# Optimization experiments

Measured on AMD Instinct MI355X. Metric: run time of the kernel, lower is better.

## Reference

```python
import jax, jax.numpy as jnp
import numpy as np

N, E, IN_DIM, HID, HEADS, OUT_DIM, MAX_N = 40000, 200000, 32, 64, 4, 32, 8
SLOPE = 0.2  # GATv2Conv default negative_slope


def setup_inputs() -> dict:
    key = jax.random.key(0)
    ks = jax.random.split(key, 10)
    s = lambda k, shape: jax.random.normal(k, shape, dtype=jnp.float32) * 0.1
    return {
        "feat": jax.random.normal(ks[0], (N, IN_DIM), dtype=jnp.float32),
        "edge_index": jax.random.randint(ks[1], (2, E), 0, N, dtype=jnp.int32),
        # edge_mask values in 1..MAX_N so max().item() == MAX_N as in the torch loop
        "edge_mask": jax.random.randint(ks[2], (E,), 1, MAX_N + 1, dtype=jnp.int32),
        "current_state": jnp.ones((N,), dtype=jnp.bool_),
        "W_in": s(ks[3], (HID, IN_DIM)), "b_in": jnp.zeros((HID,), jnp.float32),
        "W_l": s(ks[4], (HEADS * HID, 2 * HID)), "b_l": jnp.zeros((HEADS * HID,), jnp.float32),
        "W_r": s(ks[5], (HEADS * HID, 2 * HID)), "b_r": jnp.zeros((HEADS * HID,), jnp.float32),
        "att": s(ks[6], (HEADS, HID)),
        "b_conv": jnp.zeros((HEADS * HID,), jnp.float32),
        "W_g": s(ks[7], (OUT_DIM, HID)), "b_g": jnp.zeros((OUT_DIM,), jnp.float32),
    }


def _gatv2(x, src, dst, emask, W_l, b_l, W_r, b_r, att, b_conv):
    """GATv2Conv(2*HID -> HID, heads=HEADS, add_self_loops=False) on masked edges."""
    xl = (x @ W_l.T + b_l).reshape(N, HEADS, HID)  # source transform
    xr = (x @ W_r.T + b_r).reshape(N, HEADS, HID)  # target transform
    e = jax.nn.leaky_relu(xl[src] + xr[dst], SLOPE)          # (E, heads, hid)
    logits = jnp.einsum('ehd,hd->eh', e, att)                # (E, heads)
    logits = jnp.where(emask[:, None], logits, -1e9)
    seg_max = jax.ops.segment_max(logits, dst, num_segments=N)
    w = jnp.exp(logits - seg_max[dst]) * emask[:, None].astype(logits.dtype)
    denom = jax.ops.segment_sum(w, dst, num_segments=N)
    alpha = w / jnp.maximum(denom[dst], 1e-16)               # scatter-softmax over dst
    out = jax.ops.segment_sum(xl[src] * alpha[:, :, None], dst, num_segments=N)
    return out + b_conv.reshape(HEADS, HID)                  # (N, heads, hid)


def reference(feat, edge_index, edge_mask, current_state, W_in, b_in,
              W_l, b_l, W_r, b_r, att, b_conv, W_g, b_g):
    src, dst = edge_index[0], edge_index[1]
    h0 = feat @ W_in.T + b_in
    h = h0
    temp = jnp.zeros_like(h)
    for i in range(MAX_N):  # max_n = edge_mask.max() == MAX_N by construction
        emask = i < edge_mask
        conv = _gatv2(jnp.concatenate([h, h0], axis=1), src, dst, emask,
                      W_l, b_l, W_r, b_r, att, b_conv)
        h = jnp.tanh(conv.sum(axis=1))         # view(N, heads, hid).sum(1) then tanh
        temp = jnp.where(h != 0, h, temp)      # temp[nonzero_mask] = h[nonzero_mask]
    hg = temp[current_state]                   # all-ones mask -> (N, HID)
    return hg @ W_g.T + b_g
```

## Files before the change

### kernel.cpp

```cpp
#include <hip/hip_runtime.h>
#include <math.h>

#define HID 64
#define HEADS 4
#define IN_DIM 32
#define OUT_DIM 32
#define MAX_ITERS 8
#define SLOPE 0.2f

typedef __attribute__((ext_vector_type(8))) short short8;
typedef __attribute__((ext_vector_type(4))) float floatx4;

__device__ inline ushort f2bf(float x) {
    union { float f; uint u; } c;
    c.f = x;
    uint u = c.u;
    return (ushort)((u + 0x7fffu + ((u >> 16) & 1u)) >> 16);
}

__global__ void k_prepw(const float* __restrict__ W_l, const float* __restrict__ W_r,
                        short* __restrict__ Wb) {
    int idx = blockIdx.x * blockDim.x + threadIdx.x;
    if (idx >= 512 * 128) return;
    int o = idx >> 7, k = idx & 127;
    float v = (o < 256) ? W_l[o * 128 + k] : W_r[(o - 256) * 128 + k];
    int bn = o >> 4, olo = o & 15, ks = k >> 5, kq = (k >> 3) & 3, j = k & 7;
    int lane = kq * 16 + olo;
    Wb[(((bn * 4 + ks) * 64 + lane) << 3) + j] = (short)f2bf(v);
}

__global__ void k_prepw2(const float* __restrict__ W_in, const float* __restrict__ W_g,
                         float* __restrict__ WTin, float* __restrict__ WTg) {
    int idx = blockIdx.x * blockDim.x + threadIdx.x;
    if (idx < HID * IN_DIM) {
        int k = idx >> 6, j = idx & 63;
        WTin[idx] = W_in[j * IN_DIM + k];
    } else if (idx < 2 * HID * IN_DIM) {
        int i2 = idx - HID * IN_DIM;
        int k = i2 >> 5, j = i2 & 31;
        WTg[i2] = W_g[j * HID + k];
    }
}

__global__ void k_h0(const float4* __restrict__ feat4, const float* __restrict__ WTin,
                     const float* __restrict__ b_in, ushort* __restrict__ h0b,
                     ushort* __restrict__ hb, int n_nodes) {
    int idx = blockIdx.x * blockDim.x + threadIdx.x;
    if (idx >= n_nodes * HID) return;
    int node = idx >> 6, j = idx & 63;
    const float4* f4 = feat4 + (size_t)node * 8;
    float acc = b_in[j];
#pragma unroll
    for (int kk = 0; kk < 8; ++kk) {
        float4 f = f4[kk];
        acc = fmaf(f.x, WTin[(kk * 4 + 0) * 64 + j], acc);
        acc = fmaf(f.y, WTin[(kk * 4 + 1) * 64 + j], acc);
        acc = fmaf(f.z, WTin[(kk * 4 + 2) * 64 + j], acc);
        acc = fmaf(f.w, WTin[(kk * 4 + 3) * 64 + j], acc);
    }
    ushort b = f2bf(acc);
    h0b[idx] = b;
    hb[idx] = b;
}

__global__ void k_count2(const int* __restrict__ dst, const int* __restrict__ emask,
                         int* __restrict__ deg2, int E) {
    int e = blockIdx.x * blockDim.x + threadIdx.x;
    if (e < E) atomicAdd(&deg2[dst[e] * 8 + (8 - emask[e])], 1);
}

__global__ __launch_bounds__(256) void k_scanA(const int* __restrict__ deg2,
                                               int* __restrict__ node_excl,
                                               int* __restrict__ blk_sum, int n_nodes) {
    __shared__ int sh[256];
    int t = threadIdx.x;
    int n = blockIdx.x * 256 + t;
    int d = 0;
    if (n < n_nodes) {
        const int4* p = (const int4*)(deg2 + (size_t)n * 8);
        int4 a = p[0], b = p[1];
        d = a.x + a.y + a.z + a.w + b.x + b.y + b.z + b.w;
    }
    sh[t] = d;
    __syncthreads();
    for (int off = 1; off < 256; off <<= 1) {
        int u = (t >= off) ? sh[t - off] : 0;
        __syncthreads();
        sh[t] += u;
        __syncthreads();
    }
    if (n < n_nodes) node_excl[n] = sh[t] - d;
    if (t == 255) blk_sum[blockIdx.x] = sh[255];
}

__global__ void k_scanB(int* __restrict__ blk_sum, int nblk) {
    __shared__ int sh[256];
    int t = threadIdx.x;
    int v = (t < nblk) ? blk_sum[t] : 0;
    sh[t] = v;
    __syncthreads();
    for (int off = 1; off < 256; off <<= 1) {
        int u = (t >= off) ? sh[t - off] : 0;
        __syncthreads();
        sh[t] += u;
        __syncthreads();
    }
    if (t < nblk) blk_sum[t] = sh[t] - v;
}

__global__ __launch_bounds__(256) void k_scanC(const int* __restrict__ deg2,
                                               const int* __restrict__ node_excl,
                                               const int* __restrict__ blk_sum,
                                               int* __restrict__ Sb, int* __restrict__ cur,
                                               int n_nodes) {
    int n = blockIdx.x * 256 + threadIdx.x;
    if (n >= n_nodes) return;
    int base = blk_sum[blockIdx.x] + node_excl[n];
    const int4* p = (const int4*)(deg2 + (size_t)n * 8);
    int4 a = p[0], b = p[1];
    int c[8] = {a.x, a.y, a.z, a.w, b.x, b.y, b.z, b.w};
    int run = base;
#pragma unroll
    for (int q = 0; q < 8; ++q) {
        Sb[n * 8 + q] = run;
        cur[n * 8 + q] = run;
        run += c[q];
    }
    if (n == n_nodes - 1) Sb[n_nodes * 8] = run;
}

__global__ void k_fill2(const int* __restrict__ src, const int* __restrict__ dst,
                        const int* __restrict__ emask, int* __restrict__ cur,
                        int* __restrict__ csr_src, int E) {
    int e = blockIdx.x * blockDim.x + threadIdx.x;
    if (e >= E) return;
    int pos = atomicAdd(&cur[dst[e] * 8 + (8 - emask[e])], 1);
    csr_src[pos] = src[e];
}

__global__ __launch_bounds__(256) void k_transform_mfma(
    const ushort* __restrict__ hb, const ushort* __restrict__ h0b,
    const short* __restrict__ Wb,
    const float* __restrict__ b_l, const float* __restrict__ b_r,
    float* __restrict__ xl, float* __restrict__ xr, int n_nodes) {
    __shared__ ushort As[64][136];
    int bm = blockIdx.x;
    int t = threadIdx.x;
#pragma unroll
    for (int i = 0; i < 4; ++i) {
        int idx = t + i * 256;
        int row = idx >> 4, ch = idx & 15;
        int node = bm * 64 + row;
        uint4 v = make_uint4(0, 0, 0, 0);
        if (node < n_nodes) {
            const uint4* p = (ch < 8) ? (const uint4*)(hb + (size_t)node * 64)
                                      : (const uint4*)(h0b + (size_t)node * 64);
            v = p[ch & 7];
        }
        *(uint4*)&As[row][ch * 8] = v;
    }
    __syncthreads();

    int wave = t >> 6, lane = t & 63;
    int olo = lane & 15, quad = lane >> 4;

    short8 nfrag[4][4];
#pragma unroll
    for (int ks = 0; ks < 4; ++ks)
#pragma unroll
        for (int sm = 0; sm < 4; ++sm)
            nfrag[ks][sm] = *(const short8*)&As[sm * 16 + olo][ks * 32 + quad * 8];

#pragma unroll
    for (int bn = 0; bn < 8; ++bn) {
        int cb = bn * 4 + wave;
        int o0 = cb * 16 + quad * 4;
        float4 bias = (o0 < 256) ? *(const float4*)&b_l[o0]
                                 : *(const float4*)&b_r[o0 - 256];

        floatx4 acc[4];
#pragma unroll
        for (int sm = 0; sm < 4; ++sm) acc[sm] = (floatx4){0.f, 0.f, 0.f, 0.f};

        const short8* WbF = (const short8*)Wb + (size_t)cb * 4 * 64;
#pragma unroll
        for (int ks = 0; ks < 4; ++ks) {
            short8 wfrag = WbF[ks * 64 + lane];
#pragma unroll
            for (int sm = 0; sm < 4; ++sm)
                acc[sm] = __builtin_amdgcn_mfma_f32_16x16x32_bf16(wfrag, nfrag[ks][sm], acc[sm], 0, 0, 0);
        }
#pragma unroll
        for (int sm = 0; sm < 4; ++sm) {
            int node = bm * 64 + sm * 16 + olo;
            if (node < n_nodes) {
                float4 v = make_float4(acc[sm][0] + bias.x, acc[sm][1] + bias.y,
                                       acc[sm][2] + bias.z, acc[sm][3] + bias.w);
                if (o0 < 256) *(float4*)&xl[(size_t)node * 256 + o0] = v;
                else          *(float4*)&xr[(size_t)node * 256 + (o0 - 256)] = v;
            }
        }
    }
}

__device__ inline void edge_ls(const float4* __restrict__ xl4, int s, int lane,
                               const float4& r4, const float4& at,
                               float4& a, float& ts) {
    a = xl4[(size_t)s * 64 + lane];
    float vx = a.x + r4.x; vx = fmaxf(vx, SLOPE * vx);
    float vy = a.y + r4.y; vy = fmaxf(vy, SLOPE * vy);
    float vz = a.z + r4.z; vz = fmaxf(vz, SLOPE * vz);
    float vw = a.w + r4.w; vw = fmaxf(vw, SLOPE * vw);
    ts = fmaf(vx, at.x, fmaf(vy, at.y, fmaf(vz, at.z, vw * at.w)));
}

__global__ __launch_bounds__(256) void k_fused(
    const float4* __restrict__ xl4, const float4* __restrict__ xr4,
    const int* __restrict__ Sb, const int* __restrict__ csr_src,
    const float4* __restrict__ att4, const float* __restrict__ b_conv,
    ushort* __restrict__ hb, float* __restrict__ temp, int iter, int n_nodes) {
    int gid = blockIdx.x * blockDim.x + threadIdx.x;
    int n = __builtin_amdgcn_readfirstlane(gid >> 6);
    int lane = threadIdx.x & 63;
    if (n >= n_nodes) return;
    int p0 = Sb[n * 8];
    int p1 = Sb[n * 8 + (8 - iter)];

    float ax = 0.f, ay = 0.f, az = 0.f, aw = 0.f, denom = 0.f;
    if (p1 > p0) {
        float4 at = att4[lane];
        float4 r4 = xr4[(size_t)n * 64 + lane];
        int p = p0;
        for (; p + 4 <= p1; p += 4) {
            int s0 = csr_src[p], s1 = csr_src[p + 1], s2 = csr_src[p + 2], s3 = csr_src[p + 3];
            float4 a0, a1, a2, a3;
            float ts0, ts1, ts2, ts3;
            edge_ls(xl4, s0, lane, r4, at, a0, ts0);
            edge_ls(xl4, s1, lane, r4, at, a1, ts1);
            edge_ls(xl4, s2, lane, r4, at, a2, ts2);
            edge_ls(xl4, s3, lane, r4, at, a3, ts3);
            ts0 += __shfl_xor(ts0, 1); ts1 += __shfl_xor(ts1, 1);
            ts2 += __shfl_xor(ts2, 1); ts3 += __shfl_xor(ts3, 1);
            ts0 += __shfl_xor(ts0, 2); ts1 += __shfl_xor(ts1, 2);
            ts2 += __shfl_xor(ts2, 2); ts3 += __shfl_xor(ts3, 2);
            ts0 += __shfl_xor(ts0, 4); ts1 += __shfl_xor(ts1, 4);
            ts2 += __shfl_xor(ts2, 4); ts3 += __shfl_xor(ts3, 4);
            ts0 += __shfl_xor(ts0, 8); ts1 += __shfl_xor(ts1, 8);
            ts2 += __shfl_xor(ts2, 8); ts3 += __shfl_xor(ts3, 8);
            float w0 = __expf(ts0), w1 = __expf(ts1), w2 = __expf(ts2), w3 = __expf(ts3);
            denom += (w0 + w1) + (w2 + w3);
            ax = fmaf(w0, a0.x, fmaf(w1, a1.x, fmaf(w2, a2.x, fmaf(w3, a3.x, ax))));
            ay = fmaf(w0, a0.y, fmaf(w1, a1.y, fmaf(w2, a2.y, fmaf(w3, a3.y, ay))));
            az = fmaf(w0, a0.z, fmaf(w1, a1.z, fmaf(w2, a2.z, fmaf(w3, a3.z, az))));
            aw = fmaf(w0, a0.w, fmaf(w1, a1.w, fmaf(w2, a2.w, fmaf(w3, a3.w, aw))));
        }
        for (; p < p1; ++p) {
            int s = csr_src[p];
            float4 a;
            float ts;
            edge_ls(xl4, s, lane, r4, at, a, ts);
            ts += __shfl_xor(ts, 1);
            ts += __shfl_xor(ts, 2);
            ts += __shfl_xor(ts, 4);
            ts += __shfl_xor(ts, 8);
            float w = __expf(ts);
            denom += w;
            ax = fmaf(w, a.x, ax); ay = fmaf(w, a.y, ay);
            az = fmaf(w, a.z, az); aw = fmaf(w, a.w, aw);
        }
        float inv = 1.f / fmaxf(denom, 1e-16f);
        ax *= inv; ay *= inv; az *= inv; aw *= inv;
        ax += __shfl_xor(ax, 16); ay += __shfl_xor(ay, 16);
        az += __shfl_xor(az, 16); aw += __shfl_xor(aw, 16);
        ax += __shfl_xor(ax, 32); ay += __shfl_xor(ay, 32);
        az += __shfl_xor(az, 32); aw += __shfl_xor(aw, 32);
    }
    int dlo = (lane & 15) * 4;
    float bx = 0.f, by = 0.f, bz = 0.f, bw = 0.f;
#pragma unroll
    for (int hh = 0; hh < HEADS; ++hh) {
        bx += b_conv[hh * HID + dlo + 0];
        by += b_conv[hh * HID + dlo + 1];
        bz += b_conv[hh * HID + dlo + 2];
        bw += b_conv[hh * HID + dlo + 3];
    }
    float hx = tanhf(ax + bx), hy = tanhf(ay + by), hz = tanhf(az + bz), hw = tanhf(aw + bw);
    if (lane < 16) {
        size_t base = (size_t)n * HID + dlo;
        float4 told = *(const float4*)(temp + base);
        float4 tnew;
        tnew.x = (hx != 0.f) ? hx : told.x;
        tnew.y = (hy != 0.f) ? hy : told.y;
        tnew.z = (hz != 0.f) ? hz : told.z;
        tnew.w = (hw != 0.f) ? hw : told.w;
        *(float4*)(temp + base) = tnew;
        ushort4 hv = make_ushort4(f2bf(hx), f2bf(hy), f2bf(hz), f2bf(hw));
        *(ushort4*)(hb + base) = hv;
    }
}

__global__ void k_out(const float4* __restrict__ temp4, const float* __restrict__ WTg,
                      const float* __restrict__ b_g, float* __restrict__ out, int n_nodes) {
    int idx = blockIdx.x * blockDim.x + threadIdx.x;
    if (idx >= n_nodes * OUT_DIM) return;
    int node = idx >> 5, j = idx & 31;
    const float4* t4 = temp4 + (size_t)node * 16;
    float acc = b_g[j];
#pragma unroll
    for (int kk = 0; kk < 16; ++kk) {
        float4 t = t4[kk];
        acc = fmaf(t.x, WTg[(kk * 4 + 0) * 32 + j], acc);
        acc = fmaf(t.y, WTg[(kk * 4 + 1) * 32 + j], acc);
        acc = fmaf(t.z, WTg[(kk * 4 + 2) * 32 + j], acc);
        acc = fmaf(t.w, WTg[(kk * 4 + 3) * 32 + j], acc);
    }
    out[idx] = acc;
}

extern "C" void kernel_launch(void* const* d_in, const int* in_sizes, int n_in,
                              void* d_out, int out_size, void* d_ws, size_t ws_size,
                              hipStream_t stream) {
    const float* feat       = (const float*)d_in[0];
    const int*   edge_index = (const int*)d_in[1];
    const int*   edge_mask  = (const int*)d_in[2];
    const float* W_in   = (const float*)d_in[4];
    const float* b_in   = (const float*)d_in[5];
    const float* W_l    = (const float*)d_in[6];
    const float* b_l    = (const float*)d_in[7];
    const float* W_r    = (const float*)d_in[8];
    const float* b_r    = (const float*)d_in[9];
    const float* att    = (const float*)d_in[10];
    const float* b_conv = (const float*)d_in[11];
    const float* W_g    = (const float*)d_in[12];
    const float* b_g    = (const float*)d_in[13];
    float* out = (float*)d_out;

    const int N = in_sizes[0] / IN_DIM;
    const int E = in_sizes[1] / 2;
    const int* src = edge_index;
    const int* dst = edge_index + E;

    char* p = (char*)d_ws;
    auto alloc = [&](size_t bytes) -> char* {
        char* r = p;
        p += (bytes + 255) & ~(size_t)255;
        return r;
    };
    ushort* h0b    = (ushort*)alloc((size_t)N * HID * 2);
    ushort* hb     = (ushort*)alloc((size_t)N * HID * 2);
    float* temp    = (float*)alloc((size_t)N * HID * 4);
    float* xl      = (float*)alloc((size_t)N * HEADS * HID * 4);
    float* xr      = (float*)alloc((size_t)N * HEADS * HID * 4);
    int* deg2      = (int*)alloc((size_t)N * 8 * 4);
    int* Sb        = (int*)alloc(((size_t)N * 8 + 1) * 4);
    int* cur       = (int*)alloc((size_t)N * 8 * 4);
    int* node_excl = (int*)alloc((size_t)N * 4);
    int* blk_sum   = (int*)alloc(1024);
    int* csr_src   = (int*)alloc((size_t)E * 4);
    short* Wb      = (short*)alloc(512 * 128 * 2);
    float* WTin    = (float*)alloc(HID * IN_DIM * 4);
    float* WTg     = (float*)alloc(OUT_DIM * HID * 4);

    hipMemsetAsync(deg2, 0, (size_t)N * 8 * 4, stream);
    hipMemsetAsync(temp, 0, (size_t)N * HID * 4, stream);

    const int nblkA = (N + 255) / 256;
    k_prepw<<<(512 * 128 + 255) / 256, 256, 0, stream>>>(W_l, W_r, Wb);
    k_prepw2<<<(2 * HID * IN_DIM + 255) / 256, 256, 0, stream>>>(W_in, W_g, WTin, WTg);
    k_h0<<<(N * HID + 255) / 256, 256, 0, stream>>>((const float4*)feat, WTin, b_in, h0b, hb, N);
    k_count2<<<(E + 255) / 256, 256, 0, stream>>>(dst, edge_mask, deg2, E);
    k_scanA<<<nblkA, 256, 0, stream>>>(deg2, node_excl, blk_sum, N);
    k_scanB<<<1, 256, 0, stream>>>(blk_sum, nblkA);
    k_scanC<<<nblkA, 256, 0, stream>>>(deg2, node_excl, blk_sum, Sb, cur, N);
    k_fill2<<<(E + 255) / 256, 256, 0, stream>>>(src, dst, edge_mask, cur, csr_src, E);

    const int mblocks = (N + 63) / 64;
    for (int it = 0; it < MAX_ITERS; ++it) {
        k_transform_mfma<<<mblocks, 256, 0, stream>>>(hb, h0b, Wb, b_l, b_r, xl, xr, N);
        k_fused<<<(N + 3) / 4, 256, 0, stream>>>((const float4*)xl, (const float4*)xr,
                                                 Sb, csr_src, (const float4*)att, b_conv,
                                                 hb, temp, it, N);
    }
    k_out<<<(N * OUT_DIM + 255) / 256, 256, 0, stream>>>((const float4*)temp, WTg, b_g, out, N);
}
```

Baseline: 553.9 us.

## Fuse per-iteration aggregation with next iteration's MFMA transform using double-buffered xl/xr

Each block now aggregates 16 nodes (4 per wave), writes h and temp, then immediately runs the bf16 MFMA transform for those same 16 nodes into a second xl/xr buffer for the next iteration. The buffers ping-pong between iterations. The final iteration instead computes the output projection in the same kernel, and the setup kernels are merged (weight prep into one, h0 plus degree counting into another). This removes one launch per iteration and one read of h, at the cost of a smaller MFMA tile (16 nodes) that reloads the weights once per 16 nodes, plus twice the xl/xr workspace.

```diff
diff --git a/kernel.cpp b/kernel.cpp
--- a/kernel.cpp
+++ b/kernel.cpp
@@ -18,55 +18,59 @@
     return (ushort)((u + 0x7fffu + ((u >> 16) & 1u)) >> 16);
 }
 
-__global__ void k_prepw(const float* __restrict__ W_l, const float* __restrict__ W_r,
-                        short* __restrict__ Wb) {
+__device__ inline void edge_ls(const float4* __restrict__ xl4, int s, int lane,
+                               const float4& r4, const float4& at,
+                               float4& a, float& ts) {
+    a = xl4[(size_t)s * 64 + lane];
+    float vx = a.x + r4.x; vx = fmaxf(vx, SLOPE * vx);
+    float vy = a.y + r4.y; vy = fmaxf(vy, SLOPE * vy);
+    float vz = a.z + r4.z; vz = fmaxf(vz, SLOPE * vz);
+    float vw = a.w + r4.w; vw = fmaxf(vw, SLOPE * vw);
+    ts = fmaf(vx, at.x, fmaf(vy, at.y, fmaf(vz, at.z, vw * at.w)));
+}
+
+__global__ void k_setup0(const float* __restrict__ W_l, const float* __restrict__ W_r,
+                         const float* __restrict__ W_in, const float* __restrict__ W_g,
+                         short* __restrict__ Wb, float* __restrict__ WTin,
+                         float* __restrict__ WTg) {
+    int tid = blockIdx.x * blockDim.x + threadIdx.x;
+    int nth = gridDim.x * blockDim.x;
+    for (int idx = tid; idx < 512 * 128; idx += nth) {
+        int o = idx >> 7, k = idx & 127;
+        float v = (o < 256) ? W_l[o * 128 + k] : W_r[(o - 256) * 128 + k];
+        int cb = o >> 4, olo = o & 15, ks = k >> 5, kq = (k >> 3) & 3, j = k & 7;
+        int lane = kq * 16 + olo;
+        Wb[(((cb * 4 + ks) * 64 + lane) << 3) + j] = (short)f2bf(v);
+    }
+    for (int idx = tid; idx < 2 * HID * IN_DIM; idx += nth) {
+        if (idx < HID * IN_DIM) { int k = idx >> 6, j = idx & 63; WTin[idx] = W_in[j * IN_DIM + k]; }
+        else { int i2 = idx - HID * IN_DIM; int k = i2 >> 5, j = i2 & 31; WTg[i2] = W_g[j * HID + k]; }
+    }
+}
+
+__global__ void k_setup1(const float4* __restrict__ feat4, const float* __restrict__ WTin,
+                         const float* __restrict__ b_in, ushort* __restrict__ h0b,
+                         ushort* __restrict__ hb,
+                         const int* __restrict__ dstv, const int* __restrict__ emask,
+                         int* __restrict__ deg2, int n_nodes, int E) {
     int idx = blockIdx.x * blockDim.x + threadIdx.x;
-    if (idx >= 512 * 128) return;
-    int o = idx >> 7, k = idx & 127;
-    float v = (o < 256) ? W_l[o * 128 + k] : W_r[(o - 256) * 128 + k];
-    int bn = o >> 4, olo = o & 15, ks = k >> 5, kq = (k >> 3) & 3, j = k & 7;
-    int lane = kq * 16 + olo;
-    Wb[(((bn * 4 + ks) * 64 + lane) << 3) + j] = (short)f2bf(v);
-}
-
-__global__ void k_prepw2(const float* __restrict__ W_in, const float* __restrict__ W_g,
-                         float* __restrict__ WTin, float* __restrict__ WTg) {
-    int idx = blockIdx.x * blockDim.x + threadIdx.x;
-    if (idx < HID * IN_DIM) {
-        int k = idx >> 6, j = idx & 63;
-        WTin[idx] = W_in[j * IN_DIM + k];
-    } else if (idx < 2 * HID * IN_DIM) {
-        int i2 = idx - HID * IN_DIM;
-        int k = i2 >> 5, j = i2 & 31;
-        WTg[i2] = W_g[j * HID + k];
-    }
-}
-
-__global__ void k_h0(const float4* __restrict__ feat4, const float* __restrict__ WTin,
-                     const float* __restrict__ b_in, ushort* __restrict__ h0b,
-                     ushort* __restrict__ hb, int n_nodes) {
-    int idx = blockIdx.x * blockDim.x + threadIdx.x;
-    if (idx >= n_nodes * HID) return;
-    int node = idx >> 6, j = idx & 63;
-    const float4* f4 = feat4 + (size_t)node * 8;
-    float acc = b_in[j];
-#pragma unroll
-    for (int kk = 0; kk < 8; ++kk) {
-        float4 f = f4[kk];
-        acc = fmaf(f.x, WTin[(kk * 4 + 0) * 64 + j], acc);
-        acc = fmaf(f.y, WTin[(kk * 4 + 1) * 64 + j], acc);
-        acc = fmaf(f.z, WTin[(kk * 4 + 2) * 64 + j], acc);
-        acc = fmaf(f.w, WTin[(kk * 4 + 3) * 64 + j], acc);
-    }
-    ushort b = f2bf(acc);
-    h0b[idx] = b;
-    hb[idx] = b;
-}
-
-__global__ void k_count2(const int* __restrict__ dst, const int* __restrict__ emask,
-                         int* __restrict__ deg2, int E) {
-    int e = blockIdx.x * blockDim.x + threadIdx.x;
-    if (e < E) atomicAdd(&deg2[dst[e] * 8 + (8 - emask[e])], 1);
+    if (idx < n_nodes * HID) {
+        int node = idx >> 6, j = idx & 63;
+        const float4* f4 = feat4 + (size_t)node * 8;
+        float acc = b_in[j];
+#pragma unroll
+        for (int kk = 0; kk < 8; ++kk) {
+            float4 f = f4[kk];
+            acc = fmaf(f.x, WTin[(kk * 4 + 0) * 64 + j], acc);
+            acc = fmaf(f.y, WTin[(kk * 4 + 1) * 64 + j], acc);
+            acc = fmaf(f.z, WTin[(kk * 4 + 2) * 64 + j], acc);
+            acc = fmaf(f.w, WTin[(kk * 4 + 3) * 64 + j], acc);
+        }
+        ushort b = f2bf(acc);
+        h0b[idx] = b;
+        hb[idx] = b;
+    }
+    if (idx < E) atomicAdd(&deg2[dstv[idx] * 8 + (8 - emask[idx])], 1);
 }
 
 __global__ __launch_bounds__(256) void k_scanA(const int* __restrict__ deg2,
@@ -177,11 +181,9 @@
         int o0 = cb * 16 + quad * 4;
         float4 bias = (o0 < 256) ? *(const float4*)&b_l[o0]
                                  : *(const float4*)&b_r[o0 - 256];
-
         floatx4 acc[4];
 #pragma unroll
         for (int sm = 0; sm < 4; ++sm) acc[sm] = (floatx4){0.f, 0.f, 0.f, 0.f};
-
         const short8* WbF = (const short8*)Wb + (size_t)cb * 4 * 64;
 #pragma unroll
         for (int ks = 0; ks < 4; ++ks) {
@@ -203,118 +205,160 @@
     }
 }
 
-__device__ inline void edge_ls(const float4* __restrict__ xl4, int s, int lane,
-                               const float4& r4, const float4& at,
-                               float4& a, float& ts) {
-    a = xl4[(size_t)s * 64 + lane];
-    float vx = a.x + r4.x; vx = fmaxf(vx, SLOPE * vx);
-    float vy = a.y + r4.y; vy = fmaxf(vy, SLOPE * vy);
-    float vz = a.z + r4.z; vz = fmaxf(vz, SLOPE * vz);
-    float vw = a.w + r4.w; vw = fmaxf(vw, SLOPE * vw);
-    ts = fmaf(vx, at.x, fmaf(vy, at.y, fmaf(vz, at.z, vw * at.w)));
-}
-
-__global__ __launch_bounds__(256) void k_fused(
-    const float4* __restrict__ xl4, const float4* __restrict__ xr4,
+__global__ __launch_bounds__(256, 6) void k_merged(
+    const float4* __restrict__ xlc4, const float4* __restrict__ xrc4,
     const int* __restrict__ Sb, const int* __restrict__ csr_src,
     const float4* __restrict__ att4, const float* __restrict__ b_conv,
-    ushort* __restrict__ hb, float* __restrict__ temp, int iter, int n_nodes) {
-    int gid = blockIdx.x * blockDim.x + threadIdx.x;
-    int n = __builtin_amdgcn_readfirstlane(gid >> 6);
-    int lane = threadIdx.x & 63;
-    if (n >= n_nodes) return;
-    int p0 = Sb[n * 8];
-    int p1 = Sb[n * 8 + (8 - iter)];
-
-    float ax = 0.f, ay = 0.f, az = 0.f, aw = 0.f, denom = 0.f;
-    if (p1 > p0) {
-        float4 at = att4[lane];
-        float4 r4 = xr4[(size_t)n * 64 + lane];
-        int p = p0;
-        for (; p + 4 <= p1; p += 4) {
-            int s0 = csr_src[p], s1 = csr_src[p + 1], s2 = csr_src[p + 2], s3 = csr_src[p + 3];
-            float4 a0, a1, a2, a3;
-            float ts0, ts1, ts2, ts3;
-            edge_ls(xl4, s0, lane, r4, at, a0, ts0);
-            edge_ls(xl4, s1, lane, r4, at, a1, ts1);
-            edge_ls(xl4, s2, lane, r4, at, a2, ts2);
-            edge_ls(xl4, s3, lane, r4, at, a3, ts3);
-            ts0 += __shfl_xor(ts0, 1); ts1 += __shfl_xor(ts1, 1);
-            ts2 += __shfl_xor(ts2, 1); ts3 += __shfl_xor(ts3, 1);
-            ts0 += __shfl_xor(ts0, 2); ts1 += __shfl_xor(ts1, 2);
-            ts2 += __shfl_xor(ts2, 2); ts3 += __shfl_xor(ts3, 2);
-            ts0 += __shfl_xor(ts0, 4); ts1 += __shfl_xor(ts1, 4);
-            ts2 += __shfl_xor(ts2, 4); ts3 += __shfl_xor(ts3, 4);
-            ts0 += __shfl_xor(ts0, 8); ts1 += __shfl_xor(ts1, 8);
-            ts2 += __shfl_xor(ts2, 8); ts3 += __shfl_xor(ts3, 8);
-            float w0 = __expf(ts0), w1 = __expf(ts1), w2 = __expf(ts2), w3 = __expf(ts3);
-            denom += (w0 + w1) + (w2 + w3);
-            ax = fmaf(w0, a0.x, fmaf(w1, a1.x, fmaf(w2, a2.x, fmaf(w3, a3.x, ax))));
-            ay = fmaf(w0, a0.y, fmaf(w1, a1.y, fmaf(w2, a2.y, fmaf(w3, a3.y, ay))));
-            az = fmaf(w0, a0.z, fmaf(w1, a1.z, fmaf(w2, a2.z, fmaf(w3, a3.z, az))));
-            aw = fmaf(w0, a0.w, fmaf(w1, a1.w, fmaf(w2, a2.w, fmaf(w3, a3.w, aw))));
-        }
-        for (; p < p1; ++p) {
-            int s = csr_src[p];
-            float4 a;
-            float ts;
-            edge_ls(xl4, s, lane, r4, at, a, ts);
-            ts += __shfl_xor(ts, 1);
-            ts += __shfl_xor(ts, 2);
-            ts += __shfl_xor(ts, 4);
-            ts += __shfl_xor(ts, 8);
-            float w = __expf(ts);
-            denom += w;
-            ax = fmaf(w, a.x, ax); ay = fmaf(w, a.y, ay);
-            az = fmaf(w, a.z, az); aw = fmaf(w, a.w, aw);
-        }
-        float inv = 1.f / fmaxf(denom, 1e-16f);
-        ax *= inv; ay *= inv; az *= inv; aw *= inv;
-        ax += __shfl_xor(ax, 16); ay += __shfl_xor(ay, 16);
-        az += __shfl_xor(az, 16); aw += __shfl_xor(aw, 16);
-        ax += __shfl_xor(ax, 32); ay += __shfl_xor(ay, 32);
-        az += __shfl_xor(az, 32); aw += __shfl_xor(aw, 32);
-    }
-    int dlo = (lane & 15) * 4;
-    float bx = 0.f, by = 0.f, bz = 0.f, bw = 0.f;
-#pragma unroll
-    for (int hh = 0; hh < HEADS; ++hh) {
-        bx += b_conv[hh * HID + dlo + 0];
-        by += b_conv[hh * HID + dlo + 1];
-        bz += b_conv[hh * HID + dlo + 2];
-        bw += b_conv[hh * HID + dlo + 3];
-    }
-    float hx = tanhf(ax + bx), hy = tanhf(ay + by), hz = tanhf(az + bz), hw = tanhf(aw + bw);
-    if (lane < 16) {
-        size_t base = (size_t)n * HID + dlo;
-        float4 told = *(const float4*)(temp + base);
-        float4 tnew;
-        tnew.x = (hx != 0.f) ? hx : told.x;
-        tnew.y = (hy != 0.f) ? hy : told.y;
-        tnew.z = (hz != 0.f) ? hz : told.z;
-        tnew.w = (hw != 0.f) ? hw : told.w;
-        *(float4*)(temp + base) = tnew;
-        ushort4 hv = make_ushort4(f2bf(hx), f2bf(hy), f2bf(hz), f2bf(hw));
-        *(ushort4*)(hb + base) = hv;
-    }
-}
-
-__global__ void k_out(const float4* __restrict__ temp4, const float* __restrict__ WTg,
-                      const float* __restrict__ b_g, float* __restrict__ out, int n_nodes) {
-    int idx = blockIdx.x * blockDim.x + threadIdx.x;
-    if (idx >= n_nodes * OUT_DIM) return;
-    int node = idx >> 5, j = idx & 31;
-    const float4* t4 = temp4 + (size_t)node * 16;
-    float acc = b_g[j];
-#pragma unroll
-    for (int kk = 0; kk < 16; ++kk) {
-        float4 t = t4[kk];
-        acc = fmaf(t.x, WTg[(kk * 4 + 0) * 32 + j], acc);
-        acc = fmaf(t.y, WTg[(kk * 4 + 1) * 32 + j], acc);
-        acc = fmaf(t.z, WTg[(kk * 4 + 2) * 32 + j], acc);
-        acc = fmaf(t.w, WTg[(kk * 4 + 3) * 32 + j], acc);
-    }
-    out[idx] = acc;
+    ushort* __restrict__ hb, const ushort* __restrict__ h0b,
+    float* __restrict__ temp,
+    const short* __restrict__ Wb, const float* __restrict__ b_l, const float* __restrict__ b_r,
+    float* __restrict__ xln, float* __restrict__ xrn,
+    const float* __restrict__ WTg, const float* __restrict__ b_g, float* __restrict__ outp,
+    int iter, int n_nodes) {
+    __shared__ ushort As16[16][136];
+    const int t = threadIdx.x;
+    const int wave = t >> 6, lane = t & 63;
+    const int olo = lane & 15, quad = lane >> 4;
+    const int tile = blockIdx.x * 16;
+
+#pragma unroll 1
+    for (int i = 0; i < 4; ++i) {
+        int n = tile + wave * 4 + i;
+        if (n >= n_nodes) break;
+        int p0 = Sb[n * 8];
+        int p1 = Sb[n * 8 + (8 - iter)];
+        float ax = 0.f, ay = 0.f, az = 0.f, aw = 0.f, denom = 0.f;
+        if (p1 > p0) {
+            float4 at = att4[lane];
+            float4 r4 = xrc4[(size_t)n * 64 + lane];
+            int p = p0;
+            for (; p + 4 <= p1; p += 4) {
+                int s0 = csr_src[p], s1 = csr_src[p + 1], s2 = csr_src[p + 2], s3 = csr_src[p + 3];
+                float4 a0, a1, a2, a3;
+                float ts0, ts1, ts2, ts3;
+                edge_ls(xlc4, s0, lane, r4, at, a0, ts0);
+                edge_ls(xlc4, s1, lane, r4, at, a1, ts1);
+                edge_ls(xlc4, s2, lane, r4, at, a2, ts2);
+                edge_ls(xlc4, s3, lane, r4, at, a3, ts3);
+                ts0 += __shfl_xor(ts0, 1); ts1 += __shfl_xor(ts1, 1);
+                ts2 += __shfl_xor(ts2, 1); ts3 += __shfl_xor(ts3, 1);
+                ts0 += __shfl_xor(ts0, 2); ts1 += __shfl_xor(ts1, 2);
+                ts2 += __shfl_xor(ts2, 2); ts3 += __shfl_xor(ts3, 2);
+                ts0 += __shfl_xor(ts0, 4); ts1 += __shfl_xor(ts1, 4);
+                ts2 += __shfl_xor(ts2, 4); ts3 += __shfl_xor(ts3, 4);
+                ts0 += __shfl_xor(ts0, 8); ts1 += __shfl_xor(ts1, 8);
+                ts2 += __shfl_xor(ts2, 8); ts3 += __shfl_xor(ts3, 8);
+                float w0 = __expf(ts0), w1 = __expf(ts1), w2 = __expf(ts2), w3 = __expf(ts3);
+                denom += (w0 + w1) + (w2 + w3);
+                ax = fmaf(w0, a0.x, fmaf(w1, a1.x, fmaf(w2, a2.x, fmaf(w3, a3.x, ax))));
+                ay = fmaf(w0, a0.y, fmaf(w1, a1.y, fmaf(w2, a2.y, fmaf(w3, a3.y, ay))));
+                az = fmaf(w0, a0.z, fmaf(w1, a1.z, fmaf(w2, a2.z, fmaf(w3, a3.z, az))));
+                aw = fmaf(w0, a0.w, fmaf(w1, a1.w, fmaf(w2, a2.w, fmaf(w3, a3.w, aw))));
+            }
+            for (; p < p1; ++p) {
+                int s = csr_src[p];
+                float4 a;
+                float ts;
+                edge_ls(xlc4, s, lane, r4, at, a, ts);
+                ts += __shfl_xor(ts, 1);
+                ts += __shfl_xor(ts, 2);
+                ts += __shfl_xor(ts, 4);
+                ts += __shfl_xor(ts, 8);
+                float w = __expf(ts);
+                denom += w;
+                ax = fmaf(w, a.x, ax); ay = fmaf(w, a.y, ay);
+                az = fmaf(w, a.z, az); aw = fmaf(w, a.w, aw);
+            }
+            float inv = 1.f / fmaxf(denom, 1e-16f);
+            ax *= inv; ay *= inv; az *= inv; aw *= inv;
+            ax += __shfl_xor(ax, 16); ay += __shfl_xor(ay, 16);
+            az += __shfl_xor(az, 16); aw += __shfl_xor(aw, 16);
+            ax += __shfl_xor(ax, 32); ay += __shfl_xor(ay, 32);
+            az += __shfl_xor(az, 32); aw += __shfl_xor(aw, 32);
+        }
+        int dlo = olo * 4;
+        float bx = 0.f, by = 0.f, bz = 0.f, bw = 0.f;
+#pragma unroll
+        for (int hh = 0; hh < HEADS; ++hh) {
+            bx += b_conv[hh * HID + dlo + 0];
+            by += b_conv[hh * HID + dlo + 1];
+            bz += b_conv[hh * HID + dlo + 2];
+            bw += b_conv[hh * HID + dlo + 3];
+        }
+        float hx = tanhf(ax + bx), hy = tanhf(ay + by), hz = tanhf(az + bz), hw = tanhf(aw + bw);
+        if (lane < 16) {
+            size_t base = (size_t)n * HID + dlo;
+            float4 told = *(const float4*)(temp + base);
+            float4 tnew;
+            tnew.x = (hx != 0.f) ? hx : told.x;
+            tnew.y = (hy != 0.f) ? hy : told.y;
+            tnew.z = (hz != 0.f) ? hz : told.z;
+            tnew.w = (hw != 0.f) ? hw : told.w;
+            *(float4*)(temp + base) = tnew;
+            ushort4 hv = make_ushort4(f2bf(hx), f2bf(hy), f2bf(hz), f2bf(hw));
+            *(ushort4*)(hb + base) = hv;
+        }
+    }
+    __syncthreads();
+
+    if (iter < MAX_ITERS - 1) {
+        {
+            int row = t >> 4, ch = t & 15;
+            int node = tile + row;
+            uint4 v = make_uint4(0, 0, 0, 0);
+            if (node < n_nodes) {
+                const uint4* p = (ch < 8) ? (const uint4*)(hb + (size_t)node * 64)
+                                          : (const uint4*)(h0b + (size_t)node * 64);
+                v = p[ch & 7];
+            }
+            *(uint4*)&As16[row][ch * 8] = v;
+        }
+        __syncthreads();
+        short8 nf[4];
+#pragma unroll
+        for (int ks = 0; ks < 4; ++ks)
+            nf[ks] = *(const short8*)&As16[olo][ks * 32 + quad * 8];
+
+        int node2 = tile + olo;
+#pragma unroll
+        for (int c = 0; c < 8; ++c) {
+            int cb = c * 4 + wave;
+            int o0 = cb * 16 + quad * 4;
+            float4 bias = (o0 < 256) ? *(const float4*)&b_l[o0]
+                                     : *(const float4*)&b_r[o0 - 256];
+            floatx4 acc = (floatx4){0.f, 0.f, 0.f, 0.f};
+            const short8* WbF = (const short8*)Wb + (size_t)cb * 4 * 64;
+#pragma unroll
+            for (int ks = 0; ks < 4; ++ks)
+                acc = __builtin_amdgcn_mfma_f32_16x16x32_bf16(WbF[ks * 64 + lane], nf[ks], acc, 0, 0, 0);
+            if (node2 < n_nodes) {
+                float4 v = make_float4(acc[0] + bias.x, acc[1] + bias.y,
+                                       acc[2] + bias.z, acc[3] + bias.w);
+                if (o0 < 256) *(float4*)&xln[(size_t)node2 * 256 + o0] = v;
+                else          *(float4*)&xrn[(size_t)node2 * 256 + (o0 - 256)] = v;
+            }
+        }
+    } else {
+#pragma unroll
+        for (int i = 0; i < 2; ++i) {
+            int idx = t + i * 256;
+            int loc = idx >> 5, j = idx & 31;
+            int node = tile + loc;
+            if (node < n_nodes) {
+                const float4* t4 = (const float4*)temp + (size_t)node * 16;
+                float acc = b_g[j];
+#pragma unroll
+                for (int kk = 0; kk < 16; ++kk) {
+                    float4 tv = t4[kk];
+                    acc = fmaf(tv.x, WTg[(kk * 4 + 0) * 32 + j], acc);
+                    acc = fmaf(tv.y, WTg[(kk * 4 + 1) * 32 + j], acc);
+                    acc = fmaf(tv.z, WTg[(kk * 4 + 2) * 32 + j], acc);
+                    acc = fmaf(tv.w, WTg[(kk * 4 + 3) * 32 + j], acc);
+                }
+                outp[(size_t)node * OUT_DIM + j] = acc;
+            }
+        }
+    }
 }
 
 extern "C" void kernel_launch(void* const* d_in, const int* in_sizes, int n_in,
@@ -337,8 +381,8 @@
 
     const int N = in_sizes[0] / IN_DIM;
     const int E = in_sizes[1] / 2;
-    const int* src = edge_index;
-    const int* dst = edge_index + E;
+    const int* srcv = edge_index;
+    const int* dstv = edge_index + E;
 
     char* p = (char*)d_ws;
     auto alloc = [&](size_t bytes) -> char* {
@@ -349,8 +393,10 @@
     ushort* h0b    = (ushort*)alloc((size_t)N * HID * 2);
     ushort* hb     = (ushort*)alloc((size_t)N * HID * 2);
     float* temp    = (float*)alloc((size_t)N * HID * 4);
-    float* xl      = (float*)alloc((size_t)N * HEADS * HID * 4);
-    float* xr      = (float*)alloc((size_t)N * HEADS * HID * 4);
+    float* xlA     = (float*)alloc((size_t)N * HEADS * HID * 4);
+    float* xrA     = (float*)alloc((size_t)N * HEADS * HID * 4);
+    float* xlB     = (float*)alloc((size_t)N * HEADS * HID * 4);
+    float* xrB     = (float*)alloc((size_t)N * HEADS * HID * 4);
     int* deg2      = (int*)alloc((size_t)N * 8 * 4);
     int* Sb        = (int*)alloc(((size_t)N * 8 + 1) * 4);
     int* cur       = (int*)alloc((size_t)N * 8 * 4);
@@ -365,21 +411,25 @@
     hipMemsetAsync(temp, 0, (size_t)N * HID * 4, stream);
 
     const int nblkA = (N + 255) / 256;
-    k_prepw<<<(512 * 128 + 255) / 256, 256, 0, stream>>>(W_l, W_r, Wb);
-    k_prepw2<<<(2 * HID * IN_DIM + 255) / 256, 256, 0, stream>>>(W_in, W_g, WTin, WTg);
-    k_h0<<<(N * HID + 255) / 256, 256, 0, stream>>>((const float4*)feat, WTin, b_in, h0b, hb, N);
-    k_count2<<<(E + 255) / 256, 256, 0, stream>>>(dst, edge_mask, deg2, E);
+    k_setup0<<<64, 256, 0, stream>>>(W_l, W_r, W_in, W_g, Wb, WTin, WTg);
+    k_setup1<<<(N * HID + 255) / 256, 256, 0, stream>>>(
+        (const float4*)feat, WTin, b_in, h0b, hb, dstv, edge_mask, deg2, N, E);
     k_scanA<<<nblkA, 256, 0, stream>>>(deg2, node_excl, blk_sum, N);
     k_scanB<<<1, 256, 0, stream>>>(blk_sum, nblkA);
     k_scanC<<<nblkA, 256, 0, stream>>>(deg2, node_excl, blk_sum, Sb, cur, N);
-    k_fill2<<<(E + 255) / 256, 256, 0, stream>>>(src, dst, edge_mask, cur, csr_src, E);
-
-    const int mblocks = (N + 63) / 64;
+    k_fill2<<<(E + 255) / 256, 256, 0, stream>>>(srcv, dstv, edge_mask, cur, csr_src, E);
+
+    k_transform_mfma<<<(N + 63) / 64, 256, 0, stream>>>(hb, h0b, Wb, b_l, b_r, xlA, xrA, N);
+
+    float* xls[2] = {xlA, xlB};
+    float* xrs[2] = {xrA, xrB};
+    const int mb16 = (N + 15) / 16;
     for (int it = 0; it < MAX_ITERS; ++it) {
-        k_transform_mfma<<<mblocks, 256, 0, stream>>>(hb, h0b, Wb, b_l, b_r, xl, xr, N);
-        k_fused<<<(N + 3) / 4, 256, 0, stream>>>((const float4*)xl, (const float4*)xr,
-                                                 Sb, csr_src, (const float4*)att, b_conv,
-                                                 hb, temp, it, N);
-    }
-    k_out<<<(N * OUT_DIM + 255) / 256, 256, 0, stream>>>((const float4*)temp, WTg, b_g, out, N);
-}
+        int c = it & 1, nx = (it + 1) & 1;
+        k_merged<<<mb16, 256, 0, stream>>>(
+            (const float4*)xls[c], (const float4*)xrs[c], Sb, csr_src,
+            (const float4*)att, b_conv, hb, h0b, temp,
+            Wb, b_l, b_r, xls[nx], xrs[nx],
+            WTg, b_g, out, it, N);
+    }
+}
```

Result: slower. 651.7 us (+17.7%).

## Merge setup kernels, fuse output projection into last iteration, skip idle nodes

Applied to the files above, without the earlier changes.

The two memsets and four preprocessing kernels become two kernels: one zeroes buffers and reformats weights, the other computes h0 together with the degree counting. The final W_g projection moves into the last k_fused iteration using wave shuffles, so the separate k_out pass and its reread of temp go away. Middle iterations return early for nodes that had no active edges in this or the previous iteration, since their h and temp cannot change. This cuts launch count and some memory traffic, but adds branching and makes correctness depend on the skip condition.

```diff
diff --git a/kernel.cpp b/kernel.cpp
--- a/kernel.cpp
+++ b/kernel.cpp
@@ -18,55 +18,62 @@
     return (ushort)((u + 0x7fffu + ((u >> 16) & 1u)) >> 16);
 }
 
-__global__ void k_prepw(const float* __restrict__ W_l, const float* __restrict__ W_r,
-                        short* __restrict__ Wb) {
+__device__ inline void edge_ls(const float4* __restrict__ xl4, int s, int lane,
+                               const float4& r4, const float4& at,
+                               float4& a, float& ts) {
+    a = xl4[(size_t)s * 64 + lane];
+    float vx = a.x + r4.x; vx = fmaxf(vx, SLOPE * vx);
+    float vy = a.y + r4.y; vy = fmaxf(vy, SLOPE * vy);
+    float vz = a.z + r4.z; vz = fmaxf(vz, SLOPE * vz);
+    float vw = a.w + r4.w; vw = fmaxf(vw, SLOPE * vw);
+    ts = fmaf(vx, at.x, fmaf(vy, at.y, fmaf(vz, at.z, vw * at.w)));
+}
+
+__global__ void k_setup0(const float* __restrict__ W_l, const float* __restrict__ W_r,
+                         const float* __restrict__ W_in, const float* __restrict__ W_g,
+                         short* __restrict__ Wb, float* __restrict__ WTin,
+                         float* __restrict__ WTg, int* __restrict__ deg2,
+                         float* __restrict__ temp, int N) {
+    int tid = blockIdx.x * blockDim.x + threadIdx.x;
+    int nth = gridDim.x * blockDim.x;
+    for (int idx = tid; idx < 512 * 128; idx += nth) {
+        int o = idx >> 7, k = idx & 127;
+        float v = (o < 256) ? W_l[o * 128 + k] : W_r[(o - 256) * 128 + k];
+        int cb = o >> 4, olo = o & 15, ks = k >> 5, kq = (k >> 3) & 3, j = k & 7;
+        int lane = kq * 16 + olo;
+        Wb[(((cb * 4 + ks) * 64 + lane) << 3) + j] = (short)f2bf(v);
+    }
+    for (int idx = tid; idx < 2 * HID * IN_DIM; idx += nth) {
+        if (idx < HID * IN_DIM) { int k = idx >> 6, j = idx & 63; WTin[idx] = W_in[j * IN_DIM + k]; }
+        else { int i2 = idx - HID * IN_DIM; int k = i2 >> 5, j = i2 & 31; WTg[i2] = W_g[j * HID + k]; }
+    }
+    for (int i = tid; i < N * 8; i += nth) deg2[i] = 0;
+    for (int i = tid; i < N * HID; i += nth) temp[i] = 0.f;
+}
+
+__global__ void k_setup1(const float4* __restrict__ feat4, const float* __restrict__ WTin,
+                         const float* __restrict__ b_in, ushort* __restrict__ h0b,
+                         ushort* __restrict__ hb,
+                         const int* __restrict__ dstv, const int* __restrict__ emask,
+                         int* __restrict__ deg2, int n_nodes, int E) {
     int idx = blockIdx.x * blockDim.x + threadIdx.x;
-    if (idx >= 512 * 128) return;
-    int o = idx >> 7, k = idx & 127;
-    float v = (o < 256) ? W_l[o * 128 + k] : W_r[(o - 256) * 128 + k];
-    int bn = o >> 4, olo = o & 15, ks = k >> 5, kq = (k >> 3) & 3, j = k & 7;
-    int lane = kq * 16 + olo;
-    Wb[(((bn * 4 + ks) * 64 + lane) << 3) + j] = (short)f2bf(v);
-}
-
-__global__ void k_prepw2(const float* __restrict__ W_in, const float* __restrict__ W_g,
-                         float* __restrict__ WTin, float* __restrict__ WTg) {
-    int idx = blockIdx.x * blockDim.x + threadIdx.x;
-    if (idx < HID * IN_DIM) {
-        int k = idx >> 6, j = idx & 63;
-        WTin[idx] = W_in[j * IN_DIM + k];
-    } else if (idx < 2 * HID * IN_DIM) {
-        int i2 = idx - HID * IN_DIM;
-        int k = i2 >> 5, j = i2 & 31;
-        WTg[i2] = W_g[j * HID + k];
-    }
-}
-
-__global__ void k_h0(const float4* __restrict__ feat4, const float* __restrict__ WTin,
-                     const float* __restrict__ b_in, ushort* __restrict__ h0b,
-                     ushort* __restrict__ hb, int n_nodes) {
-    int idx = blockIdx.x * blockDim.x + threadIdx.x;
-    if (idx >= n_nodes * HID) return;
-    int node = idx >> 6, j = idx & 63;
-    const float4* f4 = feat4 + (size_t)node * 8;
-    float acc = b_in[j];
-#pragma unroll
-    for (int kk = 0; kk < 8; ++kk) {
-        float4 f = f4[kk];
-        acc = fmaf(f.x, WTin[(kk * 4 + 0) * 64 + j], acc);
-        acc = fmaf(f.y, WTin[(kk * 4 + 1) * 64 + j], acc);
-        acc = fmaf(f.z, WTin[(kk * 4 + 2) * 64 + j], acc);
-        acc = fmaf(f.w, WTin[(kk * 4 + 3) * 64 + j], acc);
-    }
-    ushort b = f2bf(acc);
-    h0b[idx] = b;
-    hb[idx] = b;
-}
-
-__global__ void k_count2(const int* __restrict__ dst, const int* __restrict__ emask,
-                         int* __restrict__ deg2, int E) {
-    int e = blockIdx.x * blockDim.x + threadIdx.x;
-    if (e < E) atomicAdd(&deg2[dst[e] * 8 + (8 - emask[e])], 1);
+    if (idx < n_nodes * HID) {
+        int node = idx >> 6, j = idx & 63;
+        const float4* f4 = feat4 + (size_t)node * 8;
+        float acc = b_in[j];
+#pragma unroll
+        for (int kk = 0; kk < 8; ++kk) {
+            float4 f = f4[kk];
+            acc = fmaf(f.x, WTin[(kk * 4 + 0) * 64 + j], acc);
+            acc = fmaf(f.y, WTin[(kk * 4 + 1) * 64 + j], acc);
+            acc = fmaf(f.z, WTin[(kk * 4 + 2) * 64 + j], acc);
+            acc = fmaf(f.w, WTin[(kk * 4 + 3) * 64 + j], acc);
+        }
+        ushort b = f2bf(acc);
+        h0b[idx] = b;
+        hb[idx] = b;
+    }
+    if (idx < E) atomicAdd(&deg2[dstv[idx] * 8 + (8 - emask[idx])], 1);
 }
 
 __global__ __launch_bounds__(256) void k_scanA(const int* __restrict__ deg2,
@@ -177,11 +184,9 @@
         int o0 = cb * 16 + quad * 4;
         float4 bias = (o0 < 256) ? *(const float4*)&b_l[o0]
                                  : *(const float4*)&b_r[o0 - 256];
-
         floatx4 acc[4];
 #pragma unroll
         for (int sm = 0; sm < 4; ++sm) acc[sm] = (floatx4){0.f, 0.f, 0.f, 0.f};
-
         const short8* WbF = (const short8*)Wb + (size_t)cb * 4 * 64;
 #pragma unroll
         for (int ks = 0; ks < 4; ++ks) {
@@ -203,28 +208,20 @@
     }
 }
 
-__device__ inline void edge_ls(const float4* __restrict__ xl4, int s, int lane,
-                               const float4& r4, const float4& at,
-                               float4& a, float& ts) {
-    a = xl4[(size_t)s * 64 + lane];
-    float vx = a.x + r4.x; vx = fmaxf(vx, SLOPE * vx);
-    float vy = a.y + r4.y; vy = fmaxf(vy, SLOPE * vy);
-    float vz = a.z + r4.z; vz = fmaxf(vz, SLOPE * vz);
-    float vw = a.w + r4.w; vw = fmaxf(vw, SLOPE * vw);
-    ts = fmaf(vx, at.x, fmaf(vy, at.y, fmaf(vz, at.z, vw * at.w)));
-}
-
 __global__ __launch_bounds__(256) void k_fused(
     const float4* __restrict__ xl4, const float4* __restrict__ xr4,
     const int* __restrict__ Sb, const int* __restrict__ csr_src,
     const float4* __restrict__ att4, const float* __restrict__ b_conv,
-    ushort* __restrict__ hb, float* __restrict__ temp, int iter, int n_nodes) {
+    ushort* __restrict__ hb, float* __restrict__ temp,
+    const float* __restrict__ WTg, const float* __restrict__ b_g,
+    float* __restrict__ outp, int iter, int n_nodes) {
     int gid = blockIdx.x * blockDim.x + threadIdx.x;
     int n = __builtin_amdgcn_readfirstlane(gid >> 6);
     int lane = threadIdx.x & 63;
     if (n >= n_nodes) return;
     int p0 = Sb[n * 8];
     int p1 = Sb[n * 8 + (8 - iter)];
+    if (iter > 0 && iter < MAX_ITERS - 1 && p1 == p0 && Sb[n * 8 + 9 - iter] == p0) return;
 
     float ax = 0.f, ay = 0.f, az = 0.f, aw = 0.f, denom = 0.f;
     if (p1 > p0) {
@@ -285,36 +282,42 @@
         bw += b_conv[hh * HID + dlo + 3];
     }
     float hx = tanhf(ax + bx), hy = tanhf(ay + by), hz = tanhf(az + bz), hw = tanhf(aw + bw);
-    if (lane < 16) {
+
+    if (iter < MAX_ITERS - 1) {
+        if (lane < 16) {
+            size_t base = (size_t)n * HID + dlo;
+            float4 told = *(const float4*)(temp + base);
+            float4 tnew;
+            tnew.x = (hx != 0.f) ? hx : told.x;
+            tnew.y = (hy != 0.f) ? hy : told.y;
+            tnew.z = (hz != 0.f) ? hz : told.z;
+            tnew.w = (hw != 0.f) ? hw : told.w;
+            *(float4*)(temp + base) = tnew;
+            ushort4 hv = make_ushort4(f2bf(hx), f2bf(hy), f2bf(hz), f2bf(hw));
+            *(ushort4*)(hb + base) = hv;
+        }
+    } else {
         size_t base = (size_t)n * HID + dlo;
         float4 told = *(const float4*)(temp + base);
-        float4 tnew;
-        tnew.x = (hx != 0.f) ? hx : told.x;
-        tnew.y = (hy != 0.f) ? hy : told.y;
-        tnew.z = (hz != 0.f) ? hz : told.z;
-        tnew.w = (hw != 0.f) ? hw : told.w;
-        *(float4*)(temp + base) = tnew;
-        ushort4 hv = make_ushort4(f2bf(hx), f2bf(hy), f2bf(hz), f2bf(hw));
-        *(ushort4*)(hb + base) = hv;
-    }
-}
-
-__global__ void k_out(const float4* __restrict__ temp4, const float* __restrict__ WTg,
-                      const float* __restrict__ b_g, float* __restrict__ out, int n_nodes) {
-    int idx = blockIdx.x * blockDim.x + threadIdx.x;
-    if (idx >= n_nodes * OUT_DIM) return;
-    int node = idx >> 5, j = idx & 31;
-    const float4* t4 = temp4 + (size_t)node * 16;
-    float acc = b_g[j];
-#pragma unroll
-    for (int kk = 0; kk < 16; ++kk) {
-        float4 t = t4[kk];
-        acc = fmaf(t.x, WTg[(kk * 4 + 0) * 32 + j], acc);
-        acc = fmaf(t.y, WTg[(kk * 4 + 1) * 32 + j], acc);
-        acc = fmaf(t.z, WTg[(kk * 4 + 2) * 32 + j], acc);
-        acc = fmaf(t.w, WTg[(kk * 4 + 3) * 32 + j], acc);
-    }
-    out[idx] = acc;
+        float tx = (hx != 0.f) ? hx : told.x;
+        float ty = (hy != 0.f) ? hy : told.y;
+        float tz = (hz != 0.f) ? hz : told.z;
+        float tw = (hw != 0.f) ? hw : told.w;
+        int j = lane & 31;
+        float acc = b_g[j];
+#pragma unroll
+        for (int g = 0; g < 16; ++g) {
+            float vx = __shfl(tx, g);
+            float vy = __shfl(ty, g);
+            float vz = __shfl(tz, g);
+            float vw = __shfl(tw, g);
+            acc = fmaf(vx, WTg[(g * 4 + 0) * 32 + j], acc);
+            acc = fmaf(vy, WTg[(g * 4 + 1) * 32 + j], acc);
+            acc = fmaf(vz, WTg[(g * 4 + 2) * 32 + j], acc);
+            acc = fmaf(vw, WTg[(g * 4 + 3) * 32 + j], acc);
+        }
+        if (lane < 32) outp[(size_t)n * OUT_DIM + j] = acc;
+    }
 }
 
 extern "C" void kernel_launch(void* const* d_in, const int* in_sizes, int n_in,
@@ -337,8 +340,8 @@
 
     const int N = in_sizes[0] / IN_DIM;
     const int E = in_sizes[1] / 2;
-    const int* src = edge_index;
-    const int* dst = edge_index + E;
+    const int* srcv = edge_index;
+    const int* dstv = edge_index + E;
 
     char* p = (char*)d_ws;
     auto alloc = [&](size_t bytes) -> char* {
@@ -361,25 +364,20 @@
     float* WTin    = (float*)alloc(HID * IN_DIM * 4);
     float* WTg     = (float*)alloc(OUT_DIM * HID * 4);
 
-    hipMemsetAsync(deg2, 0, (size_t)N * 8 * 4, stream);
-    hipMemsetAsync(temp, 0, (size_t)N * HID * 4, stream);
-
     const int nblkA = (N + 255) / 256;
-    k_prepw<<<(512 * 128 + 255) / 256, 256, 0, stream>>>(W_l, W_r, Wb);
-    k_prepw2<<<(2 * HID * IN_DIM + 255) / 256, 256, 0, stream>>>(W_in, W_g, WTin, WTg);
-    k_h0<<<(N * HID + 255) / 256, 256, 0, stream>>>((const float4*)feat, WTin, b_in, h0b, hb, N);
-    k_count2<<<(E + 255) / 256, 256, 0, stream>>>(dst, edge_mask, deg2, E);
+    k_setup0<<<256, 256, 0, stream>>>(W_l, W_r, W_in, W_g, Wb, WTin, WTg, deg2, temp, N);
+    k_setup1<<<(N * HID + 255) / 256, 256, 0, stream>>>(
+        (const float4*)feat, WTin, b_in, h0b, hb, dstv, edge_mask, deg2, N, E);
     k_scanA<<<nblkA, 256, 0, stream>>>(deg2, node_excl, blk_sum, N);
     k_scanB<<<1, 256, 0, stream>>>(blk_sum, nblkA);
     k_scanC<<<nblkA, 256, 0, stream>>>(deg2, node_excl, blk_sum, Sb, cur, N);
-    k_fill2<<<(E + 255) / 256, 256, 0, stream>>>(src, dst, edge_mask, cur, csr_src, E);
+    k_fill2<<<(E + 255) / 256, 256, 0, stream>>>(srcv, dstv, edge_mask, cur, csr_src, E);
 
     const int mblocks = (N + 63) / 64;
     for (int it = 0; it < MAX_ITERS; ++it) {
         k_transform_mfma<<<mblocks, 256, 0, stream>>>(hb, h0b, Wb, b_l, b_r, xl, xr, N);
         k_fused<<<(N + 3) / 4, 256, 0, stream>>>((const float4*)xl, (const float4*)xr,
                                                  Sb, csr_src, (const float4*)att, b_conv,
-                                                 hb, temp, it, N);
-    }
-    k_out<<<(N * OUT_DIM + 255) / 256, 256, 0, stream>>>((const float4*)temp, WTg, b_g, out, N);
-}
+                                                 hb, temp, WTg, b_g, out, it, N);
+    }
+}
```

After: 584.5 us. +5.5%, slower.
